# Performance work log

Hardware: AMD Instinct MI355X
Metric: run time of the kernel (lower is better)

## Reference

```python
import jax, jax.numpy as jnp
import numpy as np

D_MODEL = 768
NUM_HEADS = 12
D_K = D_MODEL // NUM_HEADS


def setup_inputs() -> dict:
    key = jax.random.key(0)
    ks = jax.random.split(key, 11)
    B, S = 2, 2048
    scale = 1.0 / np.sqrt(D_MODEL)
    inp = {
        'query': jax.random.normal(ks[0], (B, S, D_MODEL), jnp.float32),
        'key': jax.random.normal(ks[1], (B, S, D_MODEL), jnp.float32),
        'value': jax.random.normal(ks[2], (B, S, D_MODEL), jnp.float32),
        # Linear params (torch nn.Linear: y = x @ W.T + b); store as [in,out]
        'Wq': jax.random.normal(ks[3], (D_MODEL, D_MODEL), jnp.float32) * scale,
        'bq': jnp.zeros((D_MODEL,), jnp.float32),
        'Wk': jax.random.normal(ks[4], (D_MODEL, D_MODEL), jnp.float32) * scale,
        'bk': jnp.zeros((D_MODEL,), jnp.float32),
        'Wv': jax.random.normal(ks[5], (D_MODEL, D_MODEL), jnp.float32) * scale,
        'bv': jnp.zeros((D_MODEL,), jnp.float32),
        'Wo': jax.random.normal(ks[6], (D_MODEL, D_MODEL), jnp.float32) * scale,
        'bo': jnp.zeros((D_MODEL,), jnp.float32),
    }
    return inp


def _split_heads(x):
    B, S, _ = x.shape
    return x.reshape(B, S, NUM_HEADS, D_K).transpose(0, 2, 1, 3)  # [B,H,S,d_k]


def reference(query, key, value, Wq, bq, Wk, bk, Wv, bv, Wo, bo):
    q = _split_heads(query @ Wq + bq)
    k = _split_heads(key @ Wk + bk)
    v = _split_heads(value @ Wv + bv)
    scores = jnp.einsum('bhqd,bhkd->bhqk', q, k) / np.sqrt(D_K)  # [B,H,S,S]
    attn = jax.nn.softmax(scores, axis=-1)
    x = jnp.einsum('bhqk,bhkd->bhqd', attn, v)  # [B,H,S,d_k]
    B, H, S, _ = x.shape
    x = x.transpose(0, 2, 1, 3).reshape(B, S, D_MODEL)
    return x @ Wo + bo
```

## Files before the change

### kernel.cpp

```cpp
#include <hip/hip_runtime.h>
#include <hip/hip_bf16.h>

#define DM     768
#define HEADS  12
#define DK     64
#define SQ     2048
#define BATCH  2
#define ROWS   4096
#define KTILES 24

typedef __attribute__((ext_vector_type(4))) float f32x4;
typedef __bf16 bf16x8 __attribute__((ext_vector_type(8)));
typedef unsigned short u16x8 __attribute__((ext_vector_type(8)));

#define QSCALE 0.180336880f

static __device__ __forceinline__ unsigned short f2bf(float f) {
    union { float f; unsigned u; } v; v.f = f;
    unsigned u = v.u;
    unsigned lsb = (u >> 16) & 1u;
    u += 0x7fffu + lsb;
    return (unsigned short)(u >> 16);
}

static __device__ __forceinline__ unsigned pack_bf16(float a, float b) {
    __hip_bfloat162 h = __float22bfloat162_rn(make_float2(a, b));
    unsigned u;
    __builtin_memcpy(&u, &h, 4);
    return u;
}

static __device__ __forceinline__ bf16x8 load_bf16x8(const unsigned short* p) {
    u16x8 u = *(const u16x8*)p;
    return __builtin_bit_cast(bf16x8, u);
}

static __device__ __forceinline__ void gld_lds16(const unsigned short* g, unsigned short* l) {
    __builtin_amdgcn_global_load_lds((const __attribute__((address_space(1))) void*)g,
                                     (__attribute__((address_space(3))) void*)l,
                                     16, 0, 0);
}

static __device__ __forceinline__ void drain_dma() {
    asm volatile("s_waitcnt vmcnt(0)" ::: "memory");
}

__global__ __launch_bounds__(256) void cvt_frag3(const float* __restrict__ X0,
                                                 const float* __restrict__ X1,
                                                 const float* __restrict__ X2,
                                                 unsigned short* __restrict__ A0,
                                                 unsigned short* __restrict__ A1,
                                                 unsigned short* __restrict__ A2) {
    int z = blockIdx.z;
    const float* X = z == 0 ? X0 : z == 1 ? X1 : X2;
    unsigned short* A = z == 0 ? A0 : z == 1 ? A1 : A2;
    int p = blockIdx.x * 256 + threadIdx.x;
    int lane = p & 63;
    int g = p >> 6;
    int ks = g % KTILES;
    int mt = g / KTILES;
    int row = mt * 16 + (lane & 15);
    int k   = ks * 32 + (lane >> 4) * 8;
    const float* src = X + (size_t)row * DM + k;
    float4 v0 = *(const float4*)src;
    float4 v1 = *(const float4*)(src + 4);
    u16x8 o;
    o[0]=f2bf(v0.x); o[1]=f2bf(v0.y); o[2]=f2bf(v0.z); o[3]=f2bf(v0.w);
    o[4]=f2bf(v1.x); o[5]=f2bf(v1.y); o[6]=f2bf(v1.z); o[7]=f2bf(v1.w);
    *(u16x8*)(A + (size_t)p * 8) = o;
}

__global__ __launch_bounds__(256) void wt_frag4(const float* __restrict__ W0,
                                                const float* __restrict__ W1,
                                                const float* __restrict__ W2,
                                                const float* __restrict__ W3,
                                                unsigned short* __restrict__ F0,
                                                unsigned short* __restrict__ F1,
                                                unsigned short* __restrict__ F2,
                                                unsigned short* __restrict__ F3) {
    int z = blockIdx.z;
    const float* W = z == 0 ? W0 : z == 1 ? W1 : z == 2 ? W2 : W3;
    unsigned short* F = z == 0 ? F0 : z == 1 ? F1 : z == 2 ? F2 : F3;
    int p = blockIdx.x * 256 + threadIdx.x;
    int lane = p & 63;
    int t = (p >> 6) & 3;
    int g = p >> 8;
    int ks = g % KTILES;
    int nb = g / KTILES;
    int n = nb * 64 + t * 16 + (lane & 15);
    int k = ks * 32 + (lane >> 4) * 8;
    u16x8 o;
#pragma unroll
    for (int j = 0; j < 8; ++j) o[j] = f2bf(W[(size_t)(k + j) * DM + n]);
    *(u16x8*)(F + (size_t)p * 8) = o;
}

__global__ __launch_bounds__(256) void gemm_qkv(const unsigned short* __restrict__ A0,
                                                const unsigned short* __restrict__ A1,
                                                const unsigned short* __restrict__ A2,
                                                const unsigned short* __restrict__ F0,
                                                const unsigned short* __restrict__ F1,
                                                const unsigned short* __restrict__ F2,
                                                const float* __restrict__ b0,
                                                const float* __restrict__ b1,
                                                const float* __restrict__ b2,
                                                unsigned short* __restrict__ Qo,
                                                unsigned short* __restrict__ Ko,
                                                unsigned short* __restrict__ Vo) {
    __shared__ __align__(16) unsigned short ldsB[2][8192];

    int z = blockIdx.z;
    const unsigned short* A = z == 0 ? A0 : z == 1 ? A1 : A2;
    const unsigned short* F = z == 0 ? F0 : z == 1 ? F1 : F2;
    const float* bias        = z == 0 ? b0 : z == 1 ? b1 : b2;

    int w    = threadIdx.x >> 6;
    int lane = threadIdx.x & 63;
    int l15  = lane & 15;
    int quad = lane >> 4;
    int m0 = blockIdx.y * 128 + w * 32;
    int nb = blockIdx.x;
    int mt0 = m0 >> 4;

    const unsigned short* Ap = A + (size_t)mt0 * KTILES * 512 + lane * 8;
    const unsigned short* Bsrc = F + (size_t)nb * KTILES * 4 * 512 + w * 2048 + lane * 8;
    unsigned short* Bdst = &ldsB[0][w * 2048];

    f32x4 acc[2][4];
#pragma unroll
    for (int i = 0; i < 2; ++i)
#pragma unroll
        for (int t = 0; t < 4; ++t) acc[i][t] = (f32x4){0.f, 0.f, 0.f, 0.f};

#define BSTAGE(buf, c) do { \
        _Pragma("unroll") \
        for (int j = 0; j < 4; ++j) \
            gld_lds16(Bsrc + (size_t)(c) * 8192 + j * 512, Bdst + (buf) * 8192 + j * 512); \
    } while (0)

    BSTAGE(0, 0);

    for (int c = 0; c < 6; ++c) {
        drain_dma();
        __syncthreads();
        if (c < 5) BSTAGE((c + 1) & 1, c + 1);
        const unsigned short* Bl = &ldsB[c & 1][0];
#pragma unroll
        for (int k4 = 0; k4 < 4; ++k4) {
            bf16x8 a[2];
#pragma unroll
            for (int i = 0; i < 2; ++i)
                a[i] = load_bf16x8(Ap + ((size_t)i * KTILES + c * 4 + k4) * 512);
#pragma unroll
            for (int t = 0; t < 4; ++t) {
                bf16x8 bb = load_bf16x8(Bl + (k4 * 4 + t) * 512 + lane * 8);
#pragma unroll
                for (int i = 0; i < 2; ++i)
                    acc[i][t] = __builtin_amdgcn_mfma_f32_16x16x32_bf16(a[i], bb, acc[i][t], 0, 0, 0);
            }
        }
    }
#undef BSTAGE

    float scale = (z == 0) ? QSCALE : 1.0f;
#pragma unroll
    for (int t = 0; t < 4; ++t) {
        int col = nb * 64 + t * 16 + l15;
        float bv = bias[col];
        int h = col >> 6, d = col & (DK - 1);
#pragma unroll
        for (int i = 0; i < 2; ++i)
#pragma unroll
            for (int r = 0; r < 4; ++r) {
                int row = m0 + i * 16 + quad * 4 + r;
                float v = (acc[i][t][r] + bv) * scale;
                int bb = row >> 11, s = row & (SQ - 1);
                size_t bh = (size_t)(bb * HEADS + h);
                if (z == 0) {
                    Qo[(bh * SQ + s) * DK + d] = f2bf(v);
                } else if (z == 1) {
                    int sc = s & 63;
                    Ko[(bh * (SQ / 64) + (s >> 6)) * 4096 + sc * 64 +
                       (((d >> 3) ^ ((sc >> 1) & 7)) << 3) + (d & 7)] = f2bf(v);
                } else {
                    int sc = s & 63;
                    Vo[(bh * (SQ / 64) + (s >> 6)) * 4096 + d * 64 +
                       (((sc >> 3) ^ ((d >> 1) & 7)) << 3) + (sc & 7)] = f2bf(v);
                }
            }
    }
}

__global__ __launch_bounds__(256) void flash_attn(const unsigned short* __restrict__ Q,
                                                  const unsigned short* __restrict__ Kb,
                                                  const unsigned short* __restrict__ Vb,
                                                  unsigned short* __restrict__ Af) {
    __shared__ __align__(16) unsigned short ldsK[2][4096];
    __shared__ __align__(16) unsigned short ldsV[2][4096];
    __shared__ __align__(16) unsigned short ldsP[4][32 * 72];

    int w    = threadIdx.x >> 6;
    int lane = threadIdx.x & 63;
    int l15  = lane & 15;
    int quad = lane >> 4;
    int rg   = w >> 1;
    int par  = w & 1;
    int b = blockIdx.z, h = blockIdx.y;
    int q0 = blockIdx.x * 64 + rg * 32;

    size_t bh = (size_t)(b * HEADS + h);
    const unsigned short* Qp = Q  + (bh * SQ + q0) * DK;
    const unsigned short* KB = Kb + bh * (SQ / 64) * 4096;
    const unsigned short* VB = Vb + bh * (SQ / 64) * 4096;

    bf16x8 aq[2][2];
#pragma unroll
    for (int i = 0; i < 2; ++i) {
        aq[i][0] = load_bf16x8(Qp + (i * 16 + l15) * DK + quad * 8);
        aq[i][1] = load_bf16x8(Qp + (i * 16 + l15) * DK + 32 + quad * 8);
    }

    f32x4 o[2][4];
#pragma unroll
    for (int i = 0; i < 2; ++i)
#pragma unroll
        for (int t = 0; t < 4; ++t) o[i][t] = (f32x4){0.f, 0.f, 0.f, 0.f};
    float lsum[2][4] = {{0.f,0.f,0.f,0.f},{0.f,0.f,0.f,0.f}};

    unsigned short* Pw = &ldsP[w][0];

    int koff[4][2], voff[4][2];
#pragma unroll
    for (int t = 0; t < 4; ++t) {
        int pr = (t >> 1) * 32 + 2 * l15 + (t & 1);
        int sw = l15 & 7;
        koff[t][0] = pr * 64 + (((quad)     ^ sw) << 3);
        koff[t][1] = pr * 64 + (((4 + quad) ^ sw) << 3);
        int d = t * 16 + l15;
        int swv = (l15 >> 1) & 7;
        voff[t][0] = d * 64 + (((quad)     ^ swv) << 3);
        voff[t][1] = d * 64 + (((4 + quad) ^ swv) << 3);
    }

    const unsigned short* ksrc = KB + rg * 2048 + lane * 8;
    const unsigned short* vsrc = VB + rg * 2048 + lane * 8;
    unsigned short* kdst = &ldsK[par][rg * 2048];
    unsigned short* vdst = &ldsV[par][rg * 2048];

#define STAGE(n) do { \
        _Pragma("unroll") \
        for (int j = 0; j < 4; ++j) { \
            gld_lds16(ksrc + (size_t)(n) * 4096 + j * 512, kdst + j * 512); \
            gld_lds16(vsrc + (size_t)(n) * 4096 + j * 512, vdst + j * 512); \
        } \
    } while (0)

    STAGE(par);

    const unsigned short* Kl = &ldsK[par][0];
    const unsigned short* Vl = &ldsV[par][0];

    for (int s = 0; s < 16; ++s) {
        drain_dma();
        __syncthreads();

        f32x4 sc[2][4];
#pragma unroll
        for (int i = 0; i < 2; ++i)
#pragma unroll
            for (int t = 0; t < 4; ++t) sc[i][t] = (f32x4){0.f, 0.f, 0.f, 0.f};

#pragma unroll
        for (int t = 0; t < 4; ++t) {
            bf16x8 k0 = load_bf16x8(Kl + koff[t][0]);
            bf16x8 k1 = load_bf16x8(Kl + koff[t][1]);
#pragma unroll
            for (int i = 0; i < 2; ++i) {
                sc[i][t] = __builtin_amdgcn_mfma_f32_16x16x32_bf16(aq[i][0], k0, sc[i][t], 0, 0, 0);
                sc[i][t] = __builtin_amdgcn_mfma_f32_16x16x32_bf16(aq[i][1], k1, sc[i][t], 0, 0, 0);
            }
        }

#pragma unroll
        for (int i = 0; i < 2; ++i)
#pragma unroll
            for (int sub = 0; sub < 2; ++sub)
#pragma unroll
                for (int r = 0; r < 4; ++r) {
                    float e0 = exp2f(sc[i][2 * sub][r]);
                    float e1 = exp2f(sc[i][2 * sub + 1][r]);
                    lsum[i][r] += e0 + e1;
                    *(unsigned*)(Pw + (i * 16 + quad * 4 + r) * 72 + sub * 32 + l15 * 2)
                        = pack_bf16(e0, e1);
                }

        bf16x8 pf[2][2];
#pragma unroll
        for (int i = 0; i < 2; ++i) {
            pf[i][0] = load_bf16x8(Pw + (i * 16 + l15) * 72 + quad * 8);
            pf[i][1] = load_bf16x8(Pw + (i * 16 + l15) * 72 + 32 + quad * 8);
        }

#pragma unroll
        for (int t = 0; t < 4; ++t) {
            bf16x8 v0 = load_bf16x8(Vl + voff[t][0]);
            bf16x8 v1 = load_bf16x8(Vl + voff[t][1]);
#pragma unroll
            for (int i = 0; i < 2; ++i) {
                o[i][t] = __builtin_amdgcn_mfma_f32_16x16x32_bf16(pf[i][0], v0, o[i][t], 0, 0, 0);
                o[i][t] = __builtin_amdgcn_mfma_f32_16x16x32_bf16(pf[i][1], v1, o[i][t], 0, 0, 0);
            }
        }

        __syncthreads();
        if (s < 15) STAGE(2 * s + 2 + par);
    }
#undef STAGE

    float* fO = (float*)&ldsK[0][0];
    float* fL = (float*)&ldsV[0][0];
    if (par == 1) {
#pragma unroll
        for (int i = 0; i < 2; ++i)
#pragma unroll
            for (int r = 0; r < 4; ++r) {
                int rowin = i * 16 + quad * 4 + r;
#pragma unroll
                for (int t = 0; t < 4; ++t)
                    fO[rg * 2048 + rowin * 64 + t * 16 + l15] = o[i][t][r];
                fL[rg * 512 + rowin * 16 + l15] = lsum[i][r];
            }
    }
    __syncthreads();
    if (par == 0) {
#pragma unroll
        for (int i = 0; i < 2; ++i)
#pragma unroll
            for (int r = 0; r < 4; ++r) {
                int rowin = i * 16 + quad * 4 + r;
                float l = lsum[i][r] + fL[rg * 512 + rowin * 16 + l15];
                l += __shfl_xor(l, 1);
                l += __shfl_xor(l, 2);
                l += __shfl_xor(l, 4);
                l += __shfl_xor(l, 8);
                float inv = 1.0f / l;
                int R  = b * SQ + q0 + rowin;
                int mt = R >> 4;
#pragma unroll
                for (int t = 0; t < 4; ++t) {
                    float val = o[i][t][r] + fO[rg * 2048 + rowin * 64 + t * 16 + l15];
                    int ks    = h * 2 + (t >> 1);
                    int quadp = ((t & 1) << 1) + (l15 >> 3);
                    int j     = l15 & 7;
                    Af[(size_t)(mt * KTILES + ks) * 512 +
                       (size_t)((quadp << 4) + (rowin & 15)) * 8 + j] = f2bf(val * inv);
                }
            }
    }
}

__global__ __launch_bounds__(256) void gemm_out(const unsigned short* __restrict__ Af,
                                                const unsigned short* __restrict__ Ff,
                                                const float* __restrict__ bias,
                                                float* __restrict__ out) {
    __shared__ __align__(16) unsigned short ldsB[2][8192];

    int w    = threadIdx.x >> 6;
    int lane = threadIdx.x & 63;
    int l15  = lane & 15;
    int quad = lane >> 4;
    int m0 = blockIdx.y * 64 + w * 16;
    int nb = blockIdx.x;
    int mt = m0 >> 4;

    const unsigned short* Ap = Af + (size_t)mt * KTILES * 512 + lane * 8;
    const unsigned short* Bsrc = Ff + (size_t)nb * KTILES * 4 * 512 + w * 2048 + lane * 8;
    unsigned short* Bdst = &ldsB[0][w * 2048];

    f32x4 acc[4];
#pragma unroll
    for (int t = 0; t < 4; ++t) acc[t] = (f32x4){0.f, 0.f, 0.f, 0.f};

#define BSTAGE(buf, c) do { \
        _Pragma("unroll") \
        for (int j = 0; j < 4; ++j) \
            gld_lds16(Bsrc + (size_t)(c) * 8192 + j * 512, Bdst + (buf) * 8192 + j * 512); \
    } while (0)

    BSTAGE(0, 0);

    for (int c = 0; c < 6; ++c) {
        drain_dma();
        __syncthreads();
        if (c < 5) BSTAGE((c + 1) & 1, c + 1);
        const unsigned short* Bl = &ldsB[c & 1][0];
#pragma unroll
        for (int k4 = 0; k4 < 4; ++k4) {
            bf16x8 a = load_bf16x8(Ap + (size_t)(c * 4 + k4) * 512);
#pragma unroll
            for (int t = 0; t < 4; ++t) {
                bf16x8 bb = load_bf16x8(Bl + (k4 * 4 + t) * 512 + lane * 8);
                acc[t] = __builtin_amdgcn_mfma_f32_16x16x32_bf16(a, bb, acc[t], 0, 0, 0);
            }
        }
    }
#undef BSTAGE

#pragma unroll
    for (int t = 0; t < 4; ++t) {
        int col = nb * 64 + t * 16 + l15;
        float bv = bias[col];
#pragma unroll
        for (int r = 0; r < 4; ++r) {
            int row = m0 + quad * 4 + r;
            out[(size_t)row * DM + col] = acc[t][r] + bv;
        }
    }
}

extern "C" void kernel_launch(void* const* d_in, const int* in_sizes, int n_in,
                              void* d_out, int out_size, void* d_ws, size_t ws_size,
                              hipStream_t stream) {
    const float* query = (const float*)d_in[0];
    const float* key   = (const float*)d_in[1];
    const float* value = (const float*)d_in[2];
    const float* Wq = (const float*)d_in[3];  const float* bq = (const float*)d_in[4];
    const float* Wk = (const float*)d_in[5];  const float* bk = (const float*)d_in[6];
    const float* Wv = (const float*)d_in[7];  const float* bv = (const float*)d_in[8];
    const float* Wo = (const float*)d_in[9];  const float* bo = (const float*)d_in[10];

    const size_t NX = (size_t)ROWS * DM;
    const size_t NW = (size_t)DM * DM;
    unsigned short* Xq  = (unsigned short*)d_ws;
    unsigned short* Xk  = Xq  + NX;
    unsigned short* Xv  = Xk  + NX;
    unsigned short* Qb  = Xv  + NX;
    unsigned short* Kb  = Qb  + NX;
    unsigned short* Vt  = Kb  + NX;
    unsigned short* Wtq = Vt  + NX;
    unsigned short* Wtk = Wtq + NW;
    unsigned short* Wtv = Wtk + NW;
    unsigned short* Wto = Wtv + NW;

    cvt_frag3<<<dim3((unsigned)(NX / 8 / 256), 1, 3), 256, 0, stream>>>(
        query, key, value, Xq, Xk, Xv);

    wt_frag4<<<dim3((unsigned)(NW / 8 / 256), 1, 4), 256, 0, stream>>>(
        Wq, Wk, Wv, Wo, Wtq, Wtk, Wtv, Wto);

    gemm_qkv<<<dim3(DM / 64, ROWS / 128, 3), 256, 0, stream>>>(
        Xq, Xk, Xv, Wtq, Wtk, Wtv, bq, bk, bv, Qb, Kb, Vt);

    flash_attn<<<dim3(SQ / 64, HEADS, BATCH), 256, 0, stream>>>(Qb, Kb, Vt, Xq);

    gemm_out<<<dim3(DM / 64, ROWS / 64), 256, 0, stream>>>(Xq, Wto, bo, (float*)d_out);
}
```

Before: 208.3 us.

## Merge prep kernels and split each KV tile across wave pairs in attention

The two conversion kernels for activations and weights are merged into one launch with a flat block index, removing a kernel launch and its gap. In flash attention, the paired waves no longer process alternating 64-key chunks with separate buffers. Both now share each 64-key tile, each wave taking half the keys, with all four waves cooperatively double-buffering K/V loads. This brings the next tile's prefetch forward and lowers per-wave register and LDS use, at the cost of one block-wide barrier per 64-key chunk.

```diff
diff --git a/kernel.cpp b/kernel.cpp
--- a/kernel.cpp
+++ b/kernel.cpp
@@ -45,54 +45,57 @@
     asm volatile("s_waitcnt vmcnt(0)" ::: "memory");
 }
 
-__global__ __launch_bounds__(256) void cvt_frag3(const float* __restrict__ X0,
-                                                 const float* __restrict__ X1,
-                                                 const float* __restrict__ X2,
-                                                 unsigned short* __restrict__ A0,
-                                                 unsigned short* __restrict__ A1,
-                                                 unsigned short* __restrict__ A2) {
-    int z = blockIdx.z;
-    const float* X = z == 0 ? X0 : z == 1 ? X1 : X2;
-    unsigned short* A = z == 0 ? A0 : z == 1 ? A1 : A2;
-    int p = blockIdx.x * 256 + threadIdx.x;
-    int lane = p & 63;
-    int g = p >> 6;
-    int ks = g % KTILES;
-    int mt = g / KTILES;
-    int row = mt * 16 + (lane & 15);
-    int k   = ks * 32 + (lane >> 4) * 8;
-    const float* src = X + (size_t)row * DM + k;
-    float4 v0 = *(const float4*)src;
-    float4 v1 = *(const float4*)(src + 4);
-    u16x8 o;
-    o[0]=f2bf(v0.x); o[1]=f2bf(v0.y); o[2]=f2bf(v0.z); o[3]=f2bf(v0.w);
-    o[4]=f2bf(v1.x); o[5]=f2bf(v1.y); o[6]=f2bf(v1.z); o[7]=f2bf(v1.w);
-    *(u16x8*)(A + (size_t)p * 8) = o;
-}
-
-__global__ __launch_bounds__(256) void wt_frag4(const float* __restrict__ W0,
-                                                const float* __restrict__ W1,
-                                                const float* __restrict__ W2,
-                                                const float* __restrict__ W3,
-                                                unsigned short* __restrict__ F0,
-                                                unsigned short* __restrict__ F1,
-                                                unsigned short* __restrict__ F2,
-                                                unsigned short* __restrict__ F3) {
-    int z = blockIdx.z;
-    const float* W = z == 0 ? W0 : z == 1 ? W1 : z == 2 ? W2 : W3;
-    unsigned short* F = z == 0 ? F0 : z == 1 ? F1 : z == 2 ? F2 : F3;
-    int p = blockIdx.x * 256 + threadIdx.x;
-    int lane = p & 63;
-    int t = (p >> 6) & 3;
-    int g = p >> 8;
-    int ks = g % KTILES;
-    int nb = g / KTILES;
-    int n = nb * 64 + t * 16 + (lane & 15);
-    int k = ks * 32 + (lane >> 4) * 8;
-    u16x8 o;
-#pragma unroll
-    for (int j = 0; j < 8; ++j) o[j] = f2bf(W[(size_t)(k + j) * DM + n]);
-    *(u16x8*)(F + (size_t)p * 8) = o;
+__global__ __launch_bounds__(256) void prep(const float* __restrict__ Xq,
+                                            const float* __restrict__ Xk,
+                                            const float* __restrict__ Xv,
+                                            const float* __restrict__ W0,
+                                            const float* __restrict__ W1,
+                                            const float* __restrict__ W2,
+                                            const float* __restrict__ W3,
+                                            unsigned short* __restrict__ A0,
+                                            unsigned short* __restrict__ A1,
+                                            unsigned short* __restrict__ A2,
+                                            unsigned short* __restrict__ F0,
+                                            unsigned short* __restrict__ F1,
+                                            unsigned short* __restrict__ F2,
+                                            unsigned short* __restrict__ F3) {
+    int bid = blockIdx.x;
+    if (bid < 4608) {
+        int z = bid / 1536;
+        int p = (bid % 1536) * 256 + threadIdx.x;
+        const float* X = z == 0 ? Xq : z == 1 ? Xk : Xv;
+        unsigned short* A = z == 0 ? A0 : z == 1 ? A1 : A2;
+        int lane = p & 63;
+        int g = p >> 6;
+        int ks = g % KTILES;
+        int mt = g / KTILES;
+        int row = mt * 16 + (lane & 15);
+        int k   = ks * 32 + (lane >> 4) * 8;
+        const float* src = X + (size_t)row * DM + k;
+        float4 v0 = *(const float4*)src;
+        float4 v1 = *(const float4*)(src + 4);
+        u16x8 o;
+        o[0]=f2bf(v0.x); o[1]=f2bf(v0.y); o[2]=f2bf(v0.z); o[3]=f2bf(v0.w);
+        o[4]=f2bf(v1.x); o[5]=f2bf(v1.y); o[6]=f2bf(v1.z); o[7]=f2bf(v1.w);
+        *(u16x8*)(A + (size_t)p * 8) = o;
+    } else {
+        int b2 = bid - 4608;
+        int z = b2 / 288;
+        int p = (b2 % 288) * 256 + threadIdx.x;
+        const float* W = z == 0 ? W0 : z == 1 ? W1 : z == 2 ? W2 : W3;
+        unsigned short* F = z == 0 ? F0 : z == 1 ? F1 : z == 2 ? F2 : F3;
+        int lane = p & 63;
+        int t = (p >> 6) & 3;
+        int g = p >> 8;
+        int ks = g % KTILES;
+        int nb = g / KTILES;
+        int n = nb * 64 + t * 16 + (lane & 15);
+        int k = ks * 32 + (lane >> 4) * 8;
+        u16x8 o;
+#pragma unroll
+        for (int j = 0; j < 8; ++j) o[j] = f2bf(W[(size_t)(k + j) * DM + n]);
+        *(u16x8*)(F + (size_t)p * 8) = o;
+    }
 }
 
 __global__ __launch_bounds__(256) void gemm_qkv(const unsigned short* __restrict__ A0,
@@ -197,14 +200,14 @@
                                                   unsigned short* __restrict__ Af) {
     __shared__ __align__(16) unsigned short ldsK[2][4096];
     __shared__ __align__(16) unsigned short ldsV[2][4096];
-    __shared__ __align__(16) unsigned short ldsP[4][32 * 72];
+    __shared__ __align__(16) unsigned short ldsP[4][1280];
 
     int w    = threadIdx.x >> 6;
     int lane = threadIdx.x & 63;
     int l15  = lane & 15;
     int quad = lane >> 4;
     int rg   = w >> 1;
-    int par  = w & 1;
+    int kh   = w & 1;
     int b = blockIdx.z, h = blockIdx.y;
     int q0 = blockIdx.x * 64 + rg * 32;
 
@@ -229,49 +232,48 @@
 
     unsigned short* Pw = &ldsP[w][0];
 
-    int koff[4][2], voff[4][2];
-#pragma unroll
-    for (int t = 0; t < 4; ++t) {
-        int pr = (t >> 1) * 32 + 2 * l15 + (t & 1);
+    int koff[2][2], voff[4];
+#pragma unroll
+    for (int t = 0; t < 2; ++t) {
+        int pr = kh * 32 + 2 * l15 + t;
         int sw = l15 & 7;
         koff[t][0] = pr * 64 + (((quad)     ^ sw) << 3);
         koff[t][1] = pr * 64 + (((4 + quad) ^ sw) << 3);
-        int d = t * 16 + l15;
+    }
+#pragma unroll
+    for (int t = 0; t < 4; ++t) {
         int swv = (l15 >> 1) & 7;
-        voff[t][0] = d * 64 + (((quad)     ^ swv) << 3);
-        voff[t][1] = d * 64 + (((4 + quad) ^ swv) << 3);
-    }
-
-    const unsigned short* ksrc = KB + rg * 2048 + lane * 8;
-    const unsigned short* vsrc = VB + rg * 2048 + lane * 8;
-    unsigned short* kdst = &ldsK[par][rg * 2048];
-    unsigned short* vdst = &ldsV[par][rg * 2048];
-
-#define STAGE(n) do { \
-        _Pragma("unroll") \
-        for (int j = 0; j < 4; ++j) { \
-            gld_lds16(ksrc + (size_t)(n) * 4096 + j * 512, kdst + j * 512); \
-            gld_lds16(vsrc + (size_t)(n) * 4096 + j * 512, vdst + j * 512); \
-        } \
+        voff[t] = (t * 16 + l15) * 64 + ((((kh << 2) + quad) ^ swv) << 3);
+    }
+
+    const unsigned short* ksrc = KB + w * 1024 + lane * 8;
+    const unsigned short* vsrc = VB + w * 1024 + lane * 8;
+
+#define STAGE(buf, c) do { \
+        gld_lds16(ksrc + (size_t)(c) * 4096,       &ldsK[buf][w * 1024]); \
+        gld_lds16(ksrc + (size_t)(c) * 4096 + 512, &ldsK[buf][w * 1024 + 512]); \
+        gld_lds16(vsrc + (size_t)(c) * 4096,       &ldsV[buf][w * 1024]); \
+        gld_lds16(vsrc + (size_t)(c) * 4096 + 512, &ldsV[buf][w * 1024 + 512]); \
     } while (0)
 
-    STAGE(par);
-
-    const unsigned short* Kl = &ldsK[par][0];
-    const unsigned short* Vl = &ldsV[par][0];
-
-    for (int s = 0; s < 16; ++s) {
+    STAGE(0, 0);
+
+    for (int c = 0; c < SQ / 64; ++c) {
         drain_dma();
         __syncthreads();
-
-        f32x4 sc[2][4];
-#pragma unroll
-        for (int i = 0; i < 2; ++i)
-#pragma unroll
-            for (int t = 0; t < 4; ++t) sc[i][t] = (f32x4){0.f, 0.f, 0.f, 0.f};
-
-#pragma unroll
-        for (int t = 0; t < 4; ++t) {
+        if (c < SQ / 64 - 1) STAGE((c + 1) & 1, c + 1);
+
+        const unsigned short* Kl = &ldsK[c & 1][0];
+        const unsigned short* Vl = &ldsV[c & 1][0];
+
+        f32x4 sc[2][2];
+#pragma unroll
+        for (int i = 0; i < 2; ++i)
+#pragma unroll
+            for (int t = 0; t < 2; ++t) sc[i][t] = (f32x4){0.f, 0.f, 0.f, 0.f};
+
+#pragma unroll
+        for (int t = 0; t < 2; ++t) {
             bf16x8 k0 = load_bf16x8(Kl + koff[t][0]);
             bf16x8 k1 = load_bf16x8(Kl + koff[t][1]);
 #pragma unroll
@@ -284,42 +286,34 @@
 #pragma unroll
         for (int i = 0; i < 2; ++i)
 #pragma unroll
-            for (int sub = 0; sub < 2; ++sub)
-#pragma unroll
-                for (int r = 0; r < 4; ++r) {
-                    float e0 = exp2f(sc[i][2 * sub][r]);
-                    float e1 = exp2f(sc[i][2 * sub + 1][r]);
-                    lsum[i][r] += e0 + e1;
-                    *(unsigned*)(Pw + (i * 16 + quad * 4 + r) * 72 + sub * 32 + l15 * 2)
-                        = pack_bf16(e0, e1);
-                }
-
-        bf16x8 pf[2][2];
-#pragma unroll
-        for (int i = 0; i < 2; ++i) {
-            pf[i][0] = load_bf16x8(Pw + (i * 16 + l15) * 72 + quad * 8);
-            pf[i][1] = load_bf16x8(Pw + (i * 16 + l15) * 72 + 32 + quad * 8);
+            for (int r = 0; r < 4; ++r) {
+                float e0 = exp2f(sc[i][0][r]);
+                float e1 = exp2f(sc[i][1][r]);
+                lsum[i][r] += e0 + e1;
+                *(unsigned*)(Pw + (i * 16 + quad * 4 + r) * 40 + l15 * 2)
+                    = pack_bf16(e0, e1);
+            }
+
+        bf16x8 pf[2];
+#pragma unroll
+        for (int i = 0; i < 2; ++i)
+            pf[i] = load_bf16x8(Pw + (i * 16 + l15) * 40 + quad * 8);
+
+#pragma unroll
+        for (int t = 0; t < 4; ++t) {
+            bf16x8 vv = load_bf16x8(Vl + voff[t]);
+#pragma unroll
+            for (int i = 0; i < 2; ++i)
+                o[i][t] = __builtin_amdgcn_mfma_f32_16x16x32_bf16(pf[i], vv, o[i][t], 0, 0, 0);
         }
-
-#pragma unroll
-        for (int t = 0; t < 4; ++t) {
-            bf16x8 v0 = load_bf16x8(Vl + voff[t][0]);
-            bf16x8 v1 = load_bf16x8(Vl + voff[t][1]);
-#pragma unroll
-            for (int i = 0; i < 2; ++i) {
-                o[i][t] = __builtin_amdgcn_mfma_f32_16x16x32_bf16(pf[i][0], v0, o[i][t], 0, 0, 0);
-                o[i][t] = __builtin_amdgcn_mfma_f32_16x16x32_bf16(pf[i][1], v1, o[i][t], 0, 0, 0);
-            }
-        }
-
-        __syncthreads();
-        if (s < 15) STAGE(2 * s + 2 + par);
     }
 #undef STAGE
+
+    __syncthreads();
 
     float* fO = (float*)&ldsK[0][0];
     float* fL = (float*)&ldsV[0][0];
-    if (par == 1) {
+    if (kh == 1) {
 #pragma unroll
         for (int i = 0; i < 2; ++i)
 #pragma unroll
@@ -332,7 +326,7 @@
             }
     }
     __syncthreads();
-    if (par == 0) {
+    if (kh == 0) {
 #pragma unroll
         for (int i = 0; i < 2; ++i)
 #pragma unroll
@@ -442,11 +436,8 @@
     unsigned short* Wtv = Wtk + NW;
     unsigned short* Wto = Wtv + NW;
 
-    cvt_frag3<<<dim3((unsigned)(NX / 8 / 256), 1, 3), 256, 0, stream>>>(
-        query, key, value, Xq, Xk, Xv);
-
-    wt_frag4<<<dim3((unsigned)(NW / 8 / 256), 1, 4), 256, 0, stream>>>(
-        Wq, Wk, Wv, Wo, Wtq, Wtk, Wtv, Wto);
+    prep<<<5760, 256, 0, stream>>>(query, key, value, Wq, Wk, Wv, Wo,
+                                   Xq, Xk, Xv, Wtq, Wtk, Wtv, Wto);
 
     gemm_qkv<<<dim3(DM / 64, ROWS / 128, 3), 256, 0, stream>>>(
         Xq, Xk, Xv, Wtq, Wtk, Wtv, bq, bk, bv, Qb, Kb, Vt);
```

Result: slower. 213.9 us (+2.7%).
